# Kernel optimization log

Hardware: AMD Instinct MI355X
Metric: run time of the kernel (lower is better)

## Reference

```python
import jax, jax.numpy as jnp
import numpy as np

N_ITEMS = 100000
EMB = 128
LAYERS = 3
N_EDGES = 1600000


def setup_inputs() -> dict:
    key = jax.random.key(0)
    k1, k2, k3, k4, k5 = jax.random.split(key, 5)
    embedding = jax.random.normal(k1, (N_ITEMS, EMB), dtype=jnp.float32)
    adj_vals = jax.random.uniform(k2, (N_EDGES,), dtype=jnp.float32)
    # per-layer Linear(emb, emb, bias=False) weights, torch default init scale ~ 1/sqrt(fan_in)
    weights = jax.random.normal(k3, (LAYERS, EMB, EMB), dtype=jnp.float32) / np.sqrt(EMB)
    rows = jax.random.randint(k4, (N_EDGES,), 0, N_ITEMS, dtype=jnp.int32)
    cols = jax.random.randint(k5, (N_EDGES,), 0, N_ITEMS, dtype=jnp.int32)
    return {"embedding": embedding, "adj_vals": adj_vals, "weights": weights,
            "rows": rows, "cols": cols}


def reference(embedding, adj_vals, weights, rows, cols):
    n = embedding.shape[0]
    layers = weights.shape[0]
    h = embedding
    acc = embedding  # final[0] = layer-0 embedding
    for i in range(layers):
        # Linear(bias=False): x @ W^T
        h = h @ weights[i].T
        # sparse.mm: out[r] = sum_e vals[e] * h[cols[e]] for edges with rows[e]==r
        msg = adj_vals[:, None] * h[cols]            # [E, D]
        h = jax.ops.segment_sum(msg, rows, num_segments=n)  # [N, D]
        # F.normalize(p=2, dim=-1): appended to final, but the UN-normalized h feeds the next layer
        norm = jnp.maximum(jnp.sqrt(jnp.sum(h * h, axis=-1, keepdims=True)), 1e-12)
        acc = acc + h / norm
    return acc / (layers + 1)
```

## Files before the change

kernel.cpp:

```cpp
#include <hip/hip_runtime.h>

#define N_ITEMS 100000
#define EMB     128
#define N_EDGES 1600000
#define NLAYERS 3
#define NBINS   391
#define CAP_BIN 4608

typedef unsigned short u16;
typedef unsigned int   u32;
typedef __attribute__((ext_vector_type(8))) short short8;
typedef __attribute__((ext_vector_type(4))) float f32x4;

__device__ __forceinline__ float bf2f(u16 u) {
    union { u32 i; float f; } v; v.i = (u32)u << 16; return v.f;
}
__device__ __forceinline__ u16 f2bf(float f) {
    union { float f; u32 i; } v; v.f = f;
    u32 b = v.i;
    return (u16)((b + 0x7FFFu + ((b >> 16) & 1u)) >> 16);
}


__global__ __launch_bounds__(256) void fill_coarse_k(const int* __restrict__ rows,
                                                     const int* __restrict__ cols,
                                                     const float* __restrict__ vals,
                                                     int* __restrict__ bin_cnt,
                                                     int2* __restrict__ binbuf) {
    __shared__ int lcnt[NBINS];
    __shared__ int lbase[NBINS];
    int t = threadIdx.x;
    for (int d = t; d < NBINS; d += 256) lcnt[d] = 0;
    __syncthreads();
    int chunk = (N_EDGES + gridDim.x - 1) / gridDim.x;
    int e0 = blockIdx.x * chunk;
    int e1 = e0 + chunk; if (e1 > N_EDGES) e1 = N_EDGES;
    for (int e = e0 + t; e < e1; e += 256) {
        atomicAdd(&lcnt[rows[e] >> 8], 1);
    }
    __syncthreads();
    for (int d = t; d < NBINS; d += 256) {
        int c = lcnt[d];
        lbase[d] = c ? atomicAdd(&bin_cnt[d], c) : 0;
        lcnt[d] = 0;
    }
    __syncthreads();
    for (int e = e0 + t; e < e1; e += 256) {
        int r = rows[e];
        int d = r >> 8;
        int p = lbase[d] + atomicAdd(&lcnt[d], 1);
        if (p < CAP_BIN) {
            int meta = ((r & 255) << 17) | cols[e];
            binbuf[(size_t)d * CAP_BIN + p] = make_int2(meta, __float_as_int(vals[e]));
        }
    }
}


__global__ __launch_bounds__(256) void fill_fine_k(const int* __restrict__ bin_cnt,
                                                   const int2* __restrict__ binbuf,
                                                   int* __restrict__ cnt_g,
                                                   int* __restrict__ rstart_g,
                                                   int2* __restrict__ csr) {
    __shared__ int lcnt[256], loff[256], lcur[256], ltmp[256];
    int b = blockIdx.x, t = threadIdx.x;
    int ne = bin_cnt[b]; if (ne > CAP_BIN) ne = CAP_BIN;
    const int2* src = binbuf + (size_t)b * CAP_BIN;
    lcnt[t] = 0;
    __syncthreads();
    for (int i = t; i < ne; i += 256) {
        atomicAdd(&lcnt[src[i].x >> 17], 1);
    }
    __syncthreads();
    int v = lcnt[t];
    ltmp[t] = v;
    __syncthreads();
    for (int off = 1; off < 256; off <<= 1) {
        int x = (t >= off) ? ltmp[t - off] : 0;
        __syncthreads();
        ltmp[t] += x;
        __syncthreads();
    }
    loff[t] = ltmp[t] - v;
    lcur[t] = 0;
    int row = b * 256 + t;
    if (row < N_ITEMS) {
        cnt_g[row] = v;
        rstart_g[row] = b * CAP_BIN + loff[t];
    }
    __syncthreads();
    for (int i = t; i < ne; i += 256) {
        int2 ev = src[i];
        int rlow = ev.x >> 17;
        int col = ev.x & 0x1FFFF;
        int pos = loff[rlow] + atomicAdd(&lcur[rlow], 1);
        csr[(size_t)b * CAP_BIN + pos] = make_int2(col, ev.y);
    }
}


__global__ __launch_bounds__(256) void wconv_k(const float* __restrict__ W,
                                               u16* __restrict__ Wb) {
    int i = blockIdx.x * 256 + threadIdx.x;
    if (i < NLAYERS * EMB * EMB) Wb[i] = f2bf(W[i]);
}


template <bool F32IN>
__global__ __launch_bounds__(256) void gemm_k(const void* __restrict__ inp,
                                              const u16* __restrict__ Wb,
                                              u16* __restrict__ out) {
    __shared__ u16 Wl[128 * 136];
    int t = threadIdx.x;
    {
        int j = t >> 1, c0 = (t & 1) * 64;
        const short8* src = (const short8*)(Wb + j * 128 + c0);
        #pragma unroll
        for (int q = 0; q < 8; q++) {
            *(short8*)&Wl[j * 136 + c0 + q * 8] = src[q];
        }
    }
    __syncthreads();

    int l = t & 63, w = t >> 6;
    int g = l >> 4, r16 = l & 15;

    int rowA = blockIdx.x * 64 + w * 16 + r16;
    if (rowA > N_ITEMS - 1) rowA = N_ITEMS - 1;

    short8 a[4];
    if (F32IN) {
        const float* inf = (const float*)inp + (size_t)rowA * 128;
        #pragma unroll
        for (int kk = 0; kk < 4; kk++) {
            float4 p0 = *(const float4*)(inf + kk * 32 + g * 8);
            float4 p1 = *(const float4*)(inf + kk * 32 + g * 8 + 4);
            short8 s;
            s[0] = (short)f2bf(p0.x); s[1] = (short)f2bf(p0.y);
            s[2] = (short)f2bf(p0.z); s[3] = (short)f2bf(p0.w);
            s[4] = (short)f2bf(p1.x); s[5] = (short)f2bf(p1.y);
            s[6] = (short)f2bf(p1.z); s[7] = (short)f2bf(p1.w);
            a[kk] = s;
        }
    } else {
        const u16* inb = (const u16*)inp + (size_t)rowA * 128;
        #pragma unroll
        for (int kk = 0; kk < 4; kk++) {
            a[kk] = *(const short8*)(inb + kk * 32 + g * 8);
        }
    }

    int rowD0 = blockIdx.x * 64 + w * 16 + g * 4;
    #pragma unroll
    for (int jt = 0; jt < 8; jt++) {
        f32x4 acc = {0.f, 0.f, 0.f, 0.f};
        int rb = jt * 16 + r16;
        #pragma unroll
        for (int kk = 0; kk < 4; kk++) {
            short8 bfr = *(const short8*)&Wl[rb * 136 + kk * 32 + g * 8];
            acc = __builtin_amdgcn_mfma_f32_16x16x32_bf16(a[kk], bfr, acc, 0, 0, 0);
        }
        int col = jt * 16 + r16;
        #pragma unroll
        for (int i = 0; i < 4; i++) {
            int row = rowD0 + i;
            if (row < N_ITEMS) out[(size_t)row * 128 + col] = f2bf(acc[i]);
        }
    }
}


__global__ __launch_bounds__(256) void spmm_k(const u16* __restrict__ h,
                                              const int* __restrict__ rstart,
                                              const int* __restrict__ cnt,
                                              const int2* __restrict__ csr,
                                              u16* __restrict__ hn,
                                              float* __restrict__ inv) {
    int wid = (blockIdx.x * 256 + threadIdx.x) >> 6;
    int lane = threadIdx.x & 63;
    if (wid >= N_ITEMS) return;
    int s = rstart[wid];
    int n = cnt[wid];
    int2 my = make_int2(0, 0);
    if (lane < n) my = csr[(size_t)s + lane];

    const ushort2* hb = (const ushort2*)h;
    float a0 = 0.f, a1 = 0.f;
    int j = 0;
    for (; j + 4 <= n; j += 4) {
        int   c0 = __shfl(my.x, j),     c1 = __shfl(my.x, j + 1);
        int   c2 = __shfl(my.x, j + 2), c3 = __shfl(my.x, j + 3);
        float v0 = __int_as_float(__shfl(my.y, j));
        float v1 = __int_as_float(__shfl(my.y, j + 1));
        float v2 = __int_as_float(__shfl(my.y, j + 2));
        float v3 = __int_as_float(__shfl(my.y, j + 3));
        ushort2 u0 = hb[(size_t)c0 * 64 + lane];
        ushort2 u1 = hb[(size_t)c1 * 64 + lane];
        ushort2 u2 = hb[(size_t)c2 * 64 + lane];
        ushort2 u3 = hb[(size_t)c3 * 64 + lane];
        a0 += v0 * bf2f(u0.x); a1 += v0 * bf2f(u0.y);
        a0 += v1 * bf2f(u1.x); a1 += v1 * bf2f(u1.y);
        a0 += v2 * bf2f(u2.x); a1 += v2 * bf2f(u2.y);
        a0 += v3 * bf2f(u3.x); a1 += v3 * bf2f(u3.y);
    }
    for (; j < n; j++) {
        int   c0 = __shfl(my.x, j);
        float v0 = __int_as_float(__shfl(my.y, j));
        ushort2 u0 = hb[(size_t)c0 * 64 + lane];
        a0 += v0 * bf2f(u0.x); a1 += v0 * bf2f(u0.y);
    }

    float ss = a0 * a0 + a1 * a1;
    #pragma unroll
    for (int off = 32; off > 0; off >>= 1) ss += __shfl_xor(ss, off);
    ushort2 o;
    o.x = f2bf(a0);
    o.y = f2bf(a1);
    ((ushort2*)hn)[(size_t)wid * 64 + lane] = o;
    if (lane == 0) inv[wid] = 1.0f / fmaxf(sqrtf(ss), 1e-12f);
}


__global__ __launch_bounds__(256) void merge_k(const float4* __restrict__ emb4,
                                               const ushort4* __restrict__ h1,
                                               const ushort4* __restrict__ h2,
                                               const ushort4* __restrict__ h3,
                                               const float* __restrict__ inv1,
                                               const float* __restrict__ inv2,
                                               const float* __restrict__ inv3,
                                               float4* __restrict__ out4) {
    int i = blockIdx.x * 256 + threadIdx.x;
    int row = i >> 5;
    float i1 = inv1[row], i2 = inv2[row], i3 = inv3[row];
    float4 e = emb4[i];
    ushort4 a = h1[i], b = h2[i], c = h3[i];
    float4 o;
    o.x = 0.25f * (e.x + bf2f(a.x) * i1 + bf2f(b.x) * i2 + bf2f(c.x) * i3);
    o.y = 0.25f * (e.y + bf2f(a.y) * i1 + bf2f(b.y) * i2 + bf2f(c.y) * i3);
    o.z = 0.25f * (e.z + bf2f(a.z) * i1 + bf2f(b.z) * i2 + bf2f(c.z) * i3);
    o.w = 0.25f * (e.w + bf2f(a.w) * i1 + bf2f(b.w) * i2 + bf2f(c.w) * i3);
    out4[i] = o;
}


extern "C" void kernel_launch(void* const* d_in, const int* in_sizes, int n_in,
                              void* d_out, int out_size, void* d_ws, size_t ws_size,
                              hipStream_t stream) {
    const float* emb  = (const float*)d_in[0];
    const float* vals = (const float*)d_in[1];
    const float* W    = (const float*)d_in[2];
    const int*   rows = (const int*)d_in[3];
    const int*   cols = (const int*)d_in[4];
    float* out = (float*)d_out;

    char* ws = (char*)d_ws;
    size_t off = 0;
    auto alloc = [&](size_t bytes) -> void* {
        void* p = ws + off;
        off = (off + bytes + 255) & ~(size_t)255;
        return p;
    };
    size_t arena_sz = (size_t)N_ITEMS * 128 * 2;
    size_t bin_sz   = (size_t)NBINS * CAP_BIN * 8;
    char* arena = (char*)alloc(arena_sz > bin_sz ? arena_sz : bin_sz);
    int2* binbuf = (int2*)arena;
    u16*  gbuf   = (u16*)arena;

    u16*  hn0     = (u16*)alloc((size_t)N_ITEMS * 128 * 2);
    u16*  hn1     = (u16*)alloc((size_t)N_ITEMS * 128 * 2);
    u16*  hn2     = (u16*)alloc((size_t)N_ITEMS * 128 * 2);
    int2* csr     = (int2*)alloc((size_t)NBINS * CAP_BIN * 8);
    int*  bin_cnt = (int*)alloc((size_t)NBINS * 4);
    int*  cnt_g   = (int*)alloc((size_t)N_ITEMS * 4);
    int*  rstart  = (int*)alloc((size_t)N_ITEMS * 4);
    float* inv0   = (float*)alloc((size_t)N_ITEMS * 4);
    float* inv1   = (float*)alloc((size_t)N_ITEMS * 4);
    float* inv2   = (float*)alloc((size_t)N_ITEMS * 4);
    u16*  Wbf     = (u16*)alloc((size_t)NLAYERS * EMB * EMB * 2);

    hipMemsetAsync(bin_cnt, 0, (size_t)NBINS * 4, stream);
    fill_coarse_k<<<512, 256, 0, stream>>>(rows, cols, vals, bin_cnt, binbuf);
    fill_fine_k<<<NBINS, 256, 0, stream>>>(bin_cnt, binbuf, cnt_g, rstart, csr);

    wconv_k<<<(NLAYERS * EMB * EMB + 255) / 256, 256, 0, stream>>>(W, Wbf);

    u16* hn[3] = {hn0, hn1, hn2};
    float* inv[3] = {inv0, inv1, inv2};
    const void* cur = emb;
    for (int L = 0; L < NLAYERS; L++) {
        if (L == 0)
            gemm_k<true><<<(N_ITEMS + 63) / 64, 256, 0, stream>>>(cur, Wbf, gbuf);
        else
            gemm_k<false><<<(N_ITEMS + 63) / 64, 256, 0, stream>>>(cur, Wbf + (size_t)L * EMB * EMB, gbuf);
        spmm_k<<<N_ITEMS / 4, 256, 0, stream>>>(gbuf, rstart, cnt_g, csr, hn[L], inv[L]);
        cur = hn[L];
    }

    merge_k<<<(N_ITEMS * 128 / 4) / 256, 256, 0, stream>>>(
        (const float4*)emb, (const ushort4*)hn0, (const ushort4*)hn1,
        (const ushort4*)hn2, inv0, inv1, inv2, (float4*)out);
}
```

Measured before the change: 441.1 us.

## Fuse SpMM aggregation and per-layer GEMM using associativity (A·h)·Wᵀ

Reorders each layer as aggregate-then-multiply, so a single fused kernel gathers neighbor rows into shared memory (XOR-swizzled) and then runs the MFMA GEMM with the row norm computed in the epilogue. This removes the intermediate gbuf write/read and one launch per layer. The embedding is pre-converted to bf16 in a separate kernel, and column indices are pre-scaled to byte offsets. Each wave now processes 16 rows serially with half-wave edge splitting, which may lower memory-level parallelism in the gather, and the aggregate is rounded to bf16 before the GEMM.

```diff
diff --git a/kernel.cpp b/kernel.cpp
--- a/kernel.cpp
+++ b/kernel.cpp
@@ -94,7 +94,7 @@
         int rlow = ev.x >> 17;
         int col = ev.x & 0x1FFFF;
         int pos = loff[rlow] + atomicAdd(&lcur[rlow], 1);
-        csr[(size_t)b * CAP_BIN + pos] = make_int2(col, ev.y);
+        csr[(size_t)b * CAP_BIN + pos] = make_int2(col << 8, ev.y);
     }
 }
 
@@ -106,118 +106,110 @@
 }
 
 
-template <bool F32IN>
-__global__ __launch_bounds__(256) void gemm_k(const void* __restrict__ inp,
-                                              const u16* __restrict__ Wb,
-                                              u16* __restrict__ out) {
+__global__ __launch_bounds__(256) void ebf_k(const float4* __restrict__ emb,
+                                             ushort4* __restrict__ ebf) {
+    int i = blockIdx.x * 256 + threadIdx.x;
+    float4 v = emb[i];
+    ushort4 u;
+    u.x = f2bf(v.x); u.y = f2bf(v.y); u.z = f2bf(v.z); u.w = f2bf(v.w);
+    ebf[i] = u;
+}
+
+
+__global__ __launch_bounds__(256) void layer_k(const u16* __restrict__ h,
+                                               const int* __restrict__ rstart,
+                                               const int* __restrict__ cnt,
+                                               const int2* __restrict__ csr,
+                                               const u16* __restrict__ Wb,
+                                               u16* __restrict__ hn,
+                                               float* __restrict__ inv) {
     __shared__ u16 Wl[128 * 136];
+    __shared__ u16 Agg[4][16 * 128];
+
     int t = threadIdx.x;
     {
         int j = t >> 1, c0 = (t & 1) * 64;
         const short8* src = (const short8*)(Wb + j * 128 + c0);
         #pragma unroll
-        for (int q = 0; q < 8; q++) {
-            *(short8*)&Wl[j * 136 + c0 + q * 8] = src[q];
-        }
+        for (int q = 0; q < 8; q++) *(short8*)&Wl[j * 136 + c0 + q * 8] = src[q];
     }
     __syncthreads();
 
     int l = t & 63, w = t >> 6;
+    int l5 = l & 31, half = l >> 5;
+    int tileBase = blockIdx.x * 64 + w * 16;
+    char* agg = (char*)Agg[w];
+
+    for (int rr = 0; rr < 16; rr++) {
+        int row = tileBase + rr;
+        if (row > N_ITEMS - 1) row = N_ITEMS - 1;
+        int s = rstart[row], n = cnt[row];
+        int2 my = make_int2(0, 0);
+        if (l < n) my = csr[(size_t)s + l];
+        float a0 = 0.f, a1 = 0.f, a2 = 0.f, a3 = 0.f;
+        for (int j = 0; j < n; j += 4) {
+            int i0 = j + half, i1 = j + 2 + half;
+            int   c0 = __shfl(my.x, i0);
+            float v0 = __int_as_float(__shfl(my.y, i0));
+            int   c1 = __shfl(my.x, i1);
+            float v1 = __int_as_float(__shfl(my.y, i1));
+            ushort4 u0 = *(const ushort4*)((const char*)h + c0 + l5 * 8);
+            ushort4 u1 = *(const ushort4*)((const char*)h + c1 + l5 * 8);
+            a0 += v0 * bf2f(u0.x) + v1 * bf2f(u1.x);
+            a1 += v0 * bf2f(u0.y) + v1 * bf2f(u1.y);
+            a2 += v0 * bf2f(u0.z) + v1 * bf2f(u1.z);
+            a3 += v0 * bf2f(u0.w) + v1 * bf2f(u1.w);
+        }
+        a0 += __shfl_xor(a0, 32);
+        a1 += __shfl_xor(a1, 32);
+        a2 += __shfl_xor(a2, 32);
+        a3 += __shfl_xor(a3, 32);
+        if (half == 0) {
+            ushort4 o;
+            o.x = f2bf(a0); o.y = f2bf(a1); o.z = f2bf(a2); o.w = f2bf(a3);
+            int boff = (l5 * 8) ^ ((rr & 7) << 4);
+            *(ushort4*)(agg + rr * 256 + boff) = o;
+        }
+    }
+
     int g = l >> 4, r16 = l & 15;
-
-    int rowA = blockIdx.x * 64 + w * 16 + r16;
-    if (rowA > N_ITEMS - 1) rowA = N_ITEMS - 1;
-
     short8 a[4];
-    if (F32IN) {
-        const float* inf = (const float*)inp + (size_t)rowA * 128;
-        #pragma unroll
-        for (int kk = 0; kk < 4; kk++) {
-            float4 p0 = *(const float4*)(inf + kk * 32 + g * 8);
-            float4 p1 = *(const float4*)(inf + kk * 32 + g * 8 + 4);
-            short8 s;
-            s[0] = (short)f2bf(p0.x); s[1] = (short)f2bf(p0.y);
-            s[2] = (short)f2bf(p0.z); s[3] = (short)f2bf(p0.w);
-            s[4] = (short)f2bf(p1.x); s[5] = (short)f2bf(p1.y);
-            s[6] = (short)f2bf(p1.z); s[7] = (short)f2bf(p1.w);
-            a[kk] = s;
-        }
-    } else {
-        const u16* inb = (const u16*)inp + (size_t)rowA * 128;
-        #pragma unroll
-        for (int kk = 0; kk < 4; kk++) {
-            a[kk] = *(const short8*)(inb + kk * 32 + g * 8);
-        }
-    }
-
-    int rowD0 = blockIdx.x * 64 + w * 16 + g * 4;
+    #pragma unroll
+    for (int kk = 0; kk < 4; kk++) {
+        int boff = (kk * 64 + g * 16) ^ ((r16 & 7) << 4);
+        a[kk] = *(const short8*)(agg + r16 * 256 + boff);
+    }
+    int rowD0 = tileBase + g * 4;
+    float ssp[4] = {0.f, 0.f, 0.f, 0.f};
     #pragma unroll
     for (int jt = 0; jt < 8; jt++) {
         f32x4 acc = {0.f, 0.f, 0.f, 0.f};
         int rb = jt * 16 + r16;
         #pragma unroll
         for (int kk = 0; kk < 4; kk++) {
-            short8 bfr = *(const short8*)&Wl[rb * 136 + kk * 32 + g * 8];
-            acc = __builtin_amdgcn_mfma_f32_16x16x32_bf16(a[kk], bfr, acc, 0, 0, 0);
+            short8 b = *(const short8*)&Wl[rb * 136 + kk * 32 + g * 8];
+            acc = __builtin_amdgcn_mfma_f32_16x16x32_bf16(a[kk], b, acc, 0, 0, 0);
         }
         int col = jt * 16 + r16;
+        #pragma unroll
+        for (int i = 0; i < 4; i++) {
+            ssp[i] += acc[i] * acc[i];
+            int row = rowD0 + i;
+            if (row < N_ITEMS) hn[(size_t)row * 128 + col] = f2bf(acc[i]);
+        }
+    }
+    #pragma unroll
+    for (int i = 0; i < 4; i++) {
+        #pragma unroll
+        for (int off = 1; off < 16; off <<= 1) ssp[i] += __shfl_xor(ssp[i], off);
+    }
+    if (r16 == 0) {
         #pragma unroll
         for (int i = 0; i < 4; i++) {
             int row = rowD0 + i;
-            if (row < N_ITEMS) out[(size_t)row * 128 + col] = f2bf(acc[i]);
-        }
-    }
-}
-
-
-__global__ __launch_bounds__(256) void spmm_k(const u16* __restrict__ h,
-                                              const int* __restrict__ rstart,
-                                              const int* __restrict__ cnt,
-                                              const int2* __restrict__ csr,
-                                              u16* __restrict__ hn,
-                                              float* __restrict__ inv) {
-    int wid = (blockIdx.x * 256 + threadIdx.x) >> 6;
-    int lane = threadIdx.x & 63;
-    if (wid >= N_ITEMS) return;
-    int s = rstart[wid];
-    int n = cnt[wid];
-    int2 my = make_int2(0, 0);
-    if (lane < n) my = csr[(size_t)s + lane];
-
-    const ushort2* hb = (const ushort2*)h;
-    float a0 = 0.f, a1 = 0.f;
-    int j = 0;
-    for (; j + 4 <= n; j += 4) {
-        int   c0 = __shfl(my.x, j),     c1 = __shfl(my.x, j + 1);
-        int   c2 = __shfl(my.x, j + 2), c3 = __shfl(my.x, j + 3);
-        float v0 = __int_as_float(__shfl(my.y, j));
-        float v1 = __int_as_float(__shfl(my.y, j + 1));
-        float v2 = __int_as_float(__shfl(my.y, j + 2));
-        float v3 = __int_as_float(__shfl(my.y, j + 3));
-        ushort2 u0 = hb[(size_t)c0 * 64 + lane];
-        ushort2 u1 = hb[(size_t)c1 * 64 + lane];
-        ushort2 u2 = hb[(size_t)c2 * 64 + lane];
-        ushort2 u3 = hb[(size_t)c3 * 64 + lane];
-        a0 += v0 * bf2f(u0.x); a1 += v0 * bf2f(u0.y);
-        a0 += v1 * bf2f(u1.x); a1 += v1 * bf2f(u1.y);
-        a0 += v2 * bf2f(u2.x); a1 += v2 * bf2f(u2.y);
-        a0 += v3 * bf2f(u3.x); a1 += v3 * bf2f(u3.y);
-    }
-    for (; j < n; j++) {
-        int   c0 = __shfl(my.x, j);
-        float v0 = __int_as_float(__shfl(my.y, j));
-        ushort2 u0 = hb[(size_t)c0 * 64 + lane];
-        a0 += v0 * bf2f(u0.x); a1 += v0 * bf2f(u0.y);
-    }
-
-    float ss = a0 * a0 + a1 * a1;
-    #pragma unroll
-    for (int off = 32; off > 0; off >>= 1) ss += __shfl_xor(ss, off);
-    ushort2 o;
-    o.x = f2bf(a0);
-    o.y = f2bf(a1);
-    ((ushort2*)hn)[(size_t)wid * 64 + lane] = o;
-    if (lane == 0) inv[wid] = 1.0f / fmaxf(sqrtf(ss), 1e-12f);
+            if (row < N_ITEMS) inv[row] = 1.0f / fmaxf(sqrtf(ssp[i]), 1e-12f);
+        }
+    }
 }
 
 
@@ -260,11 +252,11 @@
         off = (off + bytes + 255) & ~(size_t)255;
         return p;
     };
-    size_t arena_sz = (size_t)N_ITEMS * 128 * 2;
-    size_t bin_sz   = (size_t)NBINS * CAP_BIN * 8;
-    char* arena = (char*)alloc(arena_sz > bin_sz ? arena_sz : bin_sz);
+    size_t ebf_sz = (size_t)N_ITEMS * 128 * 2;
+    size_t bin_sz = (size_t)NBINS * CAP_BIN * 8;
+    char* arena = (char*)alloc(ebf_sz > bin_sz ? ebf_sz : bin_sz);
     int2* binbuf = (int2*)arena;
-    u16*  gbuf   = (u16*)arena;
+    u16*  ebf    = (u16*)arena;
 
     u16*  hn0     = (u16*)alloc((size_t)N_ITEMS * 128 * 2);
     u16*  hn1     = (u16*)alloc((size_t)N_ITEMS * 128 * 2);
@@ -283,16 +275,15 @@
     fill_fine_k<<<NBINS, 256, 0, stream>>>(bin_cnt, binbuf, cnt_g, rstart, csr);
 
     wconv_k<<<(NLAYERS * EMB * EMB + 255) / 256, 256, 0, stream>>>(W, Wbf);
+    ebf_k<<<(N_ITEMS * 128 / 4) / 256, 256, 0, stream>>>((const float4*)emb,
+                                                         (ushort4*)ebf);
 
     u16* hn[3] = {hn0, hn1, hn2};
     float* inv[3] = {inv0, inv1, inv2};
-    const void* cur = emb;
+    const u16* cur = ebf;
     for (int L = 0; L < NLAYERS; L++) {
-        if (L == 0)
-            gemm_k<true><<<(N_ITEMS + 63) / 64, 256, 0, stream>>>(cur, Wbf, gbuf);
-        else
-            gemm_k<false><<<(N_ITEMS + 63) / 64, 256, 0, stream>>>(cur, Wbf + (size_t)L * EMB * EMB, gbuf);
-        spmm_k<<<N_ITEMS / 4, 256, 0, stream>>>(gbuf, rstart, cnt_g, csr, hn[L], inv[L]);
+        layer_k<<<(N_ITEMS + 63) / 64, 256, 0, stream>>>(
+            cur, rstart, cnt_g, csr, Wbf + (size_t)L * EMB * EMB, hn[L], inv[L]);
         cur = hn[L];
     }
 
```

New measurement: 640.5 us. 1.45x slower.
